# Kernel tuning notes

Hardware: AMD Instinct MI355X
Metric: run time of the kernel (lower is better)

The kernel has to match this reference:

```python
import jax, jax.numpy as jnp
import numpy as np
from functools import partial

B, C, FD, H, W = 8, 256, 128, 64, 64
POSC = 34  # 32 learned pos channels + 2 raw meshgrid channels


def create_meshgrid(h, w):
    # kornia-style normalized grid in [-1, 1], returned as [1, 2, h, w] (x, y)
    xs = jnp.linspace(-1.0, 1.0, w, dtype=jnp.float32)
    ys = jnp.linspace(-1.0, 1.0, h, dtype=jnp.float32)
    gy, gx = jnp.meshgrid(ys, xs, indexing='ij')
    return jnp.stack([gx, gy], axis=0)[None]  # [1,2,h,w]


def conv1x1(x, w, b):
    return jnp.einsum('bchw,oc->bohw', x, w) + b[None, :, None, None]


def pos_gen(feat, pg_w1, pg_b1, pg_w2, pg_b2):
    # PosGen type=2 with detach: two 1x1 'mul' layers (conv + ReLU, no norm)
    b, c, h, w = feat.shape
    feat = jax.lax.stop_gradient(feat)
    pos = jnp.broadcast_to(create_meshgrid(h, w), (b, 2, h, w))
    inp = jnp.concatenate([pos + 1.0, feat], axis=1)           # [b, feat_dim+2, h, w]
    h1 = jax.nn.relu(conv1x1(inp, pg_w1, pg_b1))               # [b, feat_dim, h, w]
    h2 = jax.nn.relu(conv1x1(h1, pg_w2, pg_b2))                # [b, 32, h, w]
    return jnp.concatenate([h2, pos], axis=1)                  # [b, 34, h, w]


def fuser(x, feat, w1, b1, w2, b2):
    # fuser_1D: concat along channels, 1x1 -> hidden (ReLU) -> 1x1 -> 256
    z = jnp.concatenate([x, feat], axis=1)
    z = jax.nn.relu(conv1x1(z, w1, b1))
    return conv1x1(z, w2, b2)


def conv_y(y, dw_w, dw_b, pw_w, pw_b):
    # BasicDWLayer: depthwise 3x3 + pointwise 1x1, no norm, no activation
    z = jax.lax.conv_general_dilated(
        y, dw_w, window_strides=(1, 1), padding='SAME',
        feature_group_count=y.shape[1],
        dimension_numbers=('NCHW', 'OIHW', 'NCHW')) + dw_b[None, :, None, None]
    return conv1x1(z, pw_w, pw_b)


def matching_forward(x, y, feat1, feat2,
                     pg_w1, pg_b1, pg_w2, pg_b2,
                     fus_w1, fus_b1, fus_w2, fus_b2,
                     dw_w, dw_b, pw_w, pw_b,
                     dustbin_vec, dustbin_pos):
    b, c, hx, wx = x.shape
    hy, wy = y.shape[2], y.shape[3]

    posf = pos_gen(feat2, pg_w1, pg_b1, pg_w2, pg_b2)          # [b, 34, hy, wy]
    c_pose = posf.shape[1]
    pos = posf.reshape(b, 1, c_pose, hy * wy).swapaxes(-1, -2)  # [b,1,Nk,34]

    xf = fuser(x, feat1, fus_w1, fus_b1, fus_w2, fus_b2)
    yf = fuser(y, feat2, fus_w1, fus_b1, fus_w2, fus_b2)
    yf = conv_y(yf, dw_w, dw_b, pw_w, pw_b)
    d = yf.shape[1]

    q = xf.reshape(b, 1, d, hx * wx).swapaxes(-1, -2)           # [b,1,Nq,256]
    k = yf.reshape(b, 1, d, hy * wy).swapaxes(-1, -2)           # [b,1,Nk,256]

    # dustbin token augmentation
    k = jnp.concatenate([k, jnp.broadcast_to(dustbin_vec, (b, 1, 1, d))], axis=-2)
    pos = jnp.concatenate([pos, jnp.broadcast_to(dustbin_pos, (b, 1, 1, c_pose))], axis=-2)

    # single-head cross-attention: values are the positional channels
    scores = jnp.einsum('bhqc,bhkc->bhqk', q, k) / jnp.sqrt(jnp.float32(d))
    attn = jax.nn.softmax(scores, axis=-1)
    out = jnp.einsum('bhqk,bhkd->bhqd', attn, pos)              # [b,1,Nq,34]
    return out.swapaxes(-1, -2).reshape(b, c_pose, hx, wx)


def setup_inputs() -> dict:
    key = jax.random.key(0)
    ks = jax.random.split(key, 20)
    s = 0.05
    return {
        'x': jax.random.normal(ks[0], (B, C, H, W), jnp.float32),
        'y': jax.random.normal(ks[1], (B, C, H, W), jnp.float32),
        'feat1': jax.random.normal(ks[2], (B, FD, H, W), jnp.float32),
        'feat2': jax.random.normal(ks[3], (B, FD, H, W), jnp.float32),
        # PosGen type-2 mapping: (feat_dim+2)->feat_dim, feat_dim->(hidden-2=32)
        'pg_w1': jax.random.normal(ks[4], (FD, FD + 2), jnp.float32) * s,
        'pg_b1': jnp.zeros((FD,), jnp.float32),
        'pg_w2': jax.random.normal(ks[5], (32, FD), jnp.float32) * s,
        'pg_b2': jnp.zeros((32,), jnp.float32),
        # fuser_1D: (256+128)->256 hidden, hidden->256
        'fus_w1': jax.random.normal(ks[6], (256, C + FD), jnp.float32) * s,
        'fus_b1': jnp.zeros((256,), jnp.float32),
        'fus_w2': jax.random.normal(ks[7], (C, 256), jnp.float32) * s,
        'fus_b2': jnp.zeros((C,), jnp.float32),
        # conv_y: depthwise 3x3 + pointwise 1x1
        'dw_w': jax.random.normal(ks[8], (C, 1, 3, 3), jnp.float32) * s,
        'dw_b': jnp.zeros((C,), jnp.float32),
        'pw_w': jax.random.normal(ks[9], (C, C), jnp.float32) * s,
        'pw_b': jnp.zeros((C,), jnp.float32),
        'dustbin_vec': jax.random.uniform(ks[10], (1, 1, 1, C), jnp.float32) / 10.0,
        'dustbin_pos': jnp.zeros((1, 1, 1, POSC), jnp.float32) - 10.0,
    }


def reference(x, y, feat1, feat2,
              pg_w1, pg_b1, pg_w2, pg_b2,
              fus_w1, fus_b1, fus_w2, fus_b2,
              dw_w, dw_b, pw_w, pw_b,
              dustbin_vec, dustbin_pos):
    return matching_forward(x, y, feat1, feat2,
                            pg_w1, pg_b1, pg_w2, pg_b2,
                            fus_w1, fus_b1, fus_w2, fus_b2,
                            dw_w, dw_b, pw_w, pw_b,
                            dustbin_vec, dustbin_pos)
```

## Files before the change

kernel.cpp:

```cpp
#include <hip/hip_runtime.h>
#include <hip/hip_bf16.h>

typedef __hip_bfloat16 bf16;
typedef unsigned short ushort_t;
typedef __bf16 bf16x8 __attribute__((ext_vector_type(8)));
typedef float  f32x4  __attribute__((ext_vector_type(4)));

#define HW    4096
#define NB    8
#define KSTR  4160
#define PSTR  4224
#define NTOK  32768
#define QSCALE 0.0901684400557f

__device__ __forceinline__ float lde(const void* p, size_t i, int f32f) {
    return f32f ? ((const float*)p)[i] : (float)((const bf16*)p)[i];
}
__device__ __forceinline__ ushort_t f2bu(float f){ union { __bf16 b; ushort_t u; } cv; cv.b = (__bf16)f; return cv.u; }

__global__ void detect_kernel(const ushort_t* xb, int* flag)
{
    __shared__ int cnt;
    const int t = threadIdx.x;
    if (t == 0) cnt = 0;
    __syncthreads();
    ushort_t h = xb[2*t];
    int e = (h >> 7) & 0xFF;
    if (e >= 133) atomicAdd(&cnt, 1);
    __syncthreads();
    if (t == 0) *flag = (cnt > 8) ? 1 : 0;
}

struct WsPtrs {
    bf16 *fw1t, *fw2t, *pwt, *pgw1t, *pgw2t, *dwt, *pos;
    float *posw, *fb1, *fb2, *pwb, *pgb1, *pgb2, *dwb;
};

__global__ __launch_bounds__(256) void prep_kernel(
    const void* fus_w1, const void* fus_w2, const void* pw_w,
    const void* pg_w1, const void* pg_w2, const void* dw_w,
    const void* fus_b1, const void* fus_b2, const void* pw_b,
    const void* pg_b1, const void* pg_b2, const void* dw_b,
    const void* dpos, WsPtrs W, const int* flag)
{
    const int f = *flag;
    const long n_w1 = 98304, n_w2 = 65536, n_pw = 65536, n_g1 = 16384, n_g2 = 4096;
    const long n_posw = 256, n_dwt = 2304;
    const long n_b = 256, n_gb1 = 128, n_gb2 = 32;
    const long n_mesh = 65536;
    const long n_pad  = 8L*14*PSTR;
    const long n_dust = 272;
    const long n_zt   = 8L*34*127;
    const long total = n_w1+n_w2+n_pw+n_g1+n_g2+n_posw+n_dwt
                     + 3*n_b + n_gb1 + n_gb2 + n_b + n_mesh + n_pad + n_dust + n_zt;

    for (long i = blockIdx.x*256L + threadIdx.x; i < total; i += gridDim.x*256L) {
        long j = i;
        if (j < n_w1) { W.fw1t[j] = __float2bfloat16(lde(fus_w1, j, f)); continue; } j -= n_w1;
        if (j < n_w2) { W.fw2t[j] = __float2bfloat16(lde(fus_w2, j, f)); continue; } j -= n_w2;
        if (j < n_pw) { W.pwt[j]  = __float2bfloat16(lde(pw_w,  j, f)); continue; } j -= n_pw;
        if (j < n_g1) { W.pgw1t[j] = __float2bfloat16(lde(pg_w1, (j>>7)*130 + 2 + (j&127), f)); continue; } j -= n_g1;
        if (j < n_g2) { W.pgw2t[j] = __float2bfloat16(lde(pg_w2, j, f)); continue; } j -= n_g2;
        if (j < n_posw) { W.posw[j] = lde(pg_w1, (j>>1)*130 + (j&1), f); continue; } j -= n_posw;
        if (j < n_dwt) { W.dwt[j] = __float2bfloat16(lde(dw_w, (j&255)*9 + (j>>8), f)); continue; } j -= n_dwt;
        if (j < n_b)   { W.fb1[j] = lde(fus_b1, j, f); continue; } j -= n_b;
        if (j < n_b)   { W.fb2[j] = lde(fus_b2, j, f); continue; } j -= n_b;
        if (j < n_b)   { W.pwb[j] = lde(pw_b, j, f); continue; } j -= n_b;
        if (j < n_gb1) { W.pgb1[j] = lde(pg_b1, j, f); continue; } j -= n_gb1;
        if (j < n_gb2) { W.pgb2[j] = lde(pg_b2, j, f); continue; } j -= n_gb2;
        if (j < n_b)   { W.dwb[j] = lde(dw_b, j, f); continue; } j -= n_b;
        if (j < n_mesh) {
            long b = j >> 13; int rr = (int)((j>>12)&1); int tok = (int)(j & 4095);
            float v = rr ? (-1.f + 2.f*(float)((tok>>6)&63)/63.f)
                         : (-1.f + 2.f*(float)(tok&63)/63.f);
            W.pos[((size_t)b*64 + 32 + rr)*PSTR + tok] = __float2bfloat16(v);
            continue;
        } j -= n_mesh;
        if (j < n_pad) {
            long b = j / (14L*PSTR); long rem = j % (14L*PSTR);
            int row = 34 + (int)(rem / PSTR); int tok = (int)(rem % PSTR);
            float v = (row == 34 && tok <= 4096) ? 1.f : 0.f;
            W.pos[((size_t)b*64 + row)*PSTR + tok] = __float2bfloat16(v);
            continue;
        } j -= n_pad;
        if (j < n_dust) {
            long b = j / 34; int ch = (int)(j % 34);
            W.pos[((size_t)b*64 + ch)*PSTR + 4096] = __float2bfloat16(lde(dpos, ch, f));
            continue;
        } j -= n_dust;
        { long b = j / (34*127); long rem = j % (34*127);
          int ch = (int)(rem / 127); int cc = (int)(rem % 127);
          W.pos[((size_t)b*64 + ch)*PSTR + 4097 + cc] = __float2bfloat16(0.f); }
    }
}

__global__ __launch_bounds__(256) void transpose_kernel(
    const void* main_src, const void* feat_src, bf16* __restrict__ dst, const int* flag)
{
    __shared__ float Tt[64*65];
    const int t = threadIdx.x;
    const int p0 = blockIdx.x * 64;
    const int cht = blockIdx.y;
    const int b = blockIdx.z;
    const int f = *flag;

    const void* src; int ch0, srcC, dc0;
    if (cht < 4) { src = main_src; ch0 = cht*64; srcC = 256; dc0 = ch0; }
    else         { src = feat_src; ch0 = (cht-4)*64; srcC = 128; dc0 = 256 + (cht-4)*64; }

    const int p = t & 63, cq = t >> 6;
    #pragma unroll
    for (int e = 0; e < 16; ++e) {
        int c = e*4 + cq;
        Tt[p*65 + c] = lde(src, ((size_t)b*srcC + ch0 + c)*HW + p0 + p, f);
    }
    __syncthreads();
    const int pr = t >> 2, cs = (t & 3) * 16;
    union { uint4 u4[2]; ushort_t us[16]; } pk;
    #pragma unroll
    for (int u = 0; u < 16; ++u) pk.us[u] = f2bu(Tt[pr*65 + cs + u]);
    ushort_t* op = (ushort_t*)dst + ((size_t)b*HW + p0 + pr)*384 + dc0 + cs;
    *(uint4*)op = pk.u4[0];
    *((uint4*)op + 1) = pk.u4[1];
}

template<int MT, bool RELU, bool POSEPI, int OMODE>
__global__ __launch_bounds__(256) void gemm_mfma(
    const bf16* __restrict__ A, int sa,
    const bf16* __restrict__ Bw, int ldb,
    const float* __restrict__ bias, const float* __restrict__ posw,
    bf16* __restrict__ out, int sm, int K, float oscale)
{
    const int t = threadIdx.x;
    const int w = t >> 6, lane = t & 63;
    const int n = lane & 15, quad = lane >> 4;
    const int p0 = blockIdx.x * 128;
    const int m0 = blockIdx.y * (MT*16);
    const int rowbase = p0 + w*32;

    f32x4 acc[2][MT];
    #pragma unroll
    for (int pt = 0; pt < 2; ++pt)
        #pragma unroll
        for (int mt = 0; mt < MT; ++mt) acc[pt][mt] = (f32x4){0.f,0.f,0.f,0.f};

    const bf16* Ar0 = A + (size_t)(rowbase + n)*sa + quad*8;
    const bf16* Ar1 = A + (size_t)(rowbase + 16 + n)*sa + quad*8;

    bf16x8 a0 = *(const bf16x8*)Ar0;
    bf16x8 a1 = *(const bf16x8*)Ar1;
    bf16x8 bw[MT];
    #pragma unroll
    for (int mt = 0; mt < MT; ++mt)
        bw[mt] = *(const bf16x8*)&Bw[(size_t)(m0 + mt*16 + n)*ldb + quad*8];

    const int kmax = K - 32;
    for (int k0 = 0; k0 < K; k0 += 32) {
        const int kn = (k0 < kmax) ? k0 + 32 : k0;
        bf16x8 na0 = *(const bf16x8*)(Ar0 + kn);
        bf16x8 na1 = *(const bf16x8*)(Ar1 + kn);
        bf16x8 nbw[MT];
        #pragma unroll
        for (int mt = 0; mt < MT; ++mt)
            nbw[mt] = *(const bf16x8*)&Bw[(size_t)(m0 + mt*16 + n)*ldb + kn + quad*8];
        #pragma unroll
        for (int mt = 0; mt < MT; ++mt) {
            acc[0][mt] = __builtin_amdgcn_mfma_f32_16x16x32_bf16(a0, bw[mt], acc[0][mt], 0, 0, 0);
            acc[1][mt] = __builtin_amdgcn_mfma_f32_16x16x32_bf16(a1, bw[mt], acc[1][mt], 0, 0, 0);
        }
        a0 = na0; a1 = na1;
        #pragma unroll
        for (int mt = 0; mt < MT; ++mt) bw[mt] = nbw[mt];
    }

    #pragma unroll
    for (int mt = 0; mt < MT; ++mt) {
        const int m = m0 + mt*16 + n;
        const float bi = bias[m];
        float w0 = 0.f, w1 = 0.f;
        if (POSEPI) { w0 = posw[m*2]; w1 = posw[m*2 + 1]; }
        #pragma unroll
        for (int pt = 0; pt < 2; ++pt) {
            const int tokb = rowbase + pt*16 + quad*4;
            if (OMODE == 1) {
                union { uint2 u2; ushort_t us[4]; } pk;
                #pragma unroll
                for (int r = 0; r < 4; ++r) {
                    float v = acc[pt][mt][r] + bi;
                    if (RELU) v = fmaxf(v, 0.f);
                    pk.us[r] = f2bu(v * oscale);
                }
                size_t oi = ((size_t)(tokb >> 12)*64 + m)*PSTR + (tokb & 4095);
                *(uint2*)((ushort_t*)out + oi) = pk.u2;
            } else {
                #pragma unroll
                for (int r = 0; r < 4; ++r) {
                    int tok = tokb + r;
                    float v = acc[pt][mt][r] + bi;
                    if (POSEPI) {
                        float gx1 = 2.f * (float)(tok & 63) / 63.f;
                        float gy1 = 2.f * (float)((tok >> 6) & 63) / 63.f;
                        v += w0*gx1 + w1*gy1;
                    }
                    if (RELU) v = fmaxf(v, 0.f);
                    v *= oscale;
                    size_t row = (OMODE == 2) ? (size_t)tok + 64*(size_t)(tok >> 12) : (size_t)tok;
                    out[row*sm + m] = __float2bfloat16(v);
                }
            }
        }
    }
}

__global__ __launch_bounds__(256) void dw_kernel(
    const bf16* __restrict__ in, const bf16* __restrict__ dwt,
    const float* __restrict__ dwb, bf16* __restrict__ out)
{
    const int t = threadIdx.x;
    const int tok = blockIdx.x*8 + (t >> 5);
    const int c8 = (t & 31) * 8;
    const int b = tok >> 12, p = tok & 4095;
    const int i = p >> 6, j = p & 63;

    float acc[8];
    #pragma unroll
    for (int u = 0; u < 8; ++u) acc[u] = dwb[c8 + u];

    #pragma unroll
    for (int di = 0; di < 3; ++di) {
        int ii = i + di - 1;
        if (ii < 0 || ii >= 64) continue;
        #pragma unroll
        for (int dj = 0; dj < 3; ++dj) {
            int jj = j + dj - 1;
            if (jj < 0 || jj >= 64) continue;
            int tok2 = (b << 12) + ii*64 + jj;
            bf16x8 xv = *(const bf16x8*)&in[(size_t)tok2*256 + c8];
            bf16x8 wv = *(const bf16x8*)&dwt[(di*3 + dj)*256 + c8];
            #pragma unroll
            for (int u = 0; u < 8; ++u) acc[u] += (float)xv[u] * (float)wv[u];
        }
    }
    union { uint4 u4; ushort_t us[8]; } pk;
    #pragma unroll
    for (int u = 0; u < 8; ++u) pk.us[u] = f2bu(acc[u]);
    *(uint4*)((ushort_t*)out + (size_t)tok*256 + c8) = pk.u4;
}

__global__ __launch_bounds__(256) void fill_late_kernel(
    const void* dvec, bf16* __restrict__ k_t, const int* flag)
{
    const int b = blockIdx.x, t = threadIdx.x;
    k_t[((size_t)b*KSTR + 4096)*256 + t] = __float2bfloat16(lde(dvec, t, *flag));
}

__global__ __launch_bounds__(256, 2) void attn_kernel(
    const bf16* __restrict__ q_t, const bf16* __restrict__ k_t,
    const bf16* __restrict__ pos, void* outv, const int* flag)
{
    __shared__ __align__(16) float red[4*12*64*4];
    __shared__ __align__(16) __bf16 Pb[4*64*40];

    const int t = threadIdx.x;
    const int w = t >> 6, lane = t & 63;
    const int n = lane & 15, quad = lane >> 4;
    const int qt = blockIdx.x, b = blockIdx.y;

    bf16x8 aq[4][8];
    #pragma unroll
    for (int q2 = 0; q2 < 4; ++q2) {
        size_t qrow = (size_t)b*HW + qt*64 + q2*16 + n;
        #pragma unroll
        for (int c = 0; c < 8; ++c)
            aq[q2][c] = *(const bf16x8*)&q_t[qrow*256 + c*32 + quad*8];
    }

    f32x4 pacc[4][3];
    #pragma unroll
    for (int q2 = 0; q2 < 4; ++q2)
        #pragma unroll
        for (int ct = 0; ct < 3; ++ct) pacc[q2][ct] = (f32x4){0.f,0.f,0.f,0.f};

    const bf16* kb0 = k_t + (size_t)b*KSTR*256;
    const bf16* pb0 = pos + (size_t)b*64*PSTR;
    __bf16* Pw = Pb + w*64*40;

    for (int i = 0; i < 33; ++i) {
        const int base = i*128 + w*32;

        #pragma unroll
        for (int nt2 = 0; nt2 < 2; ++nt2) {
            const int kb = base + nt2*16;
            bf16x8 bk[8];
            #pragma unroll
            for (int c = 0; c < 8; ++c)
                bk[c] = *(const bf16x8*)&kb0[(size_t)(kb + n)*256 + c*32 + quad*8];
            f32x4 sacc[4];
            #pragma unroll
            for (int q2 = 0; q2 < 4; ++q2) sacc[q2] = (f32x4){0.f,0.f,0.f,0.f};
            #pragma unroll
            for (int c = 0; c < 8; ++c)
                #pragma unroll
                for (int q2 = 0; q2 < 4; ++q2)
                    sacc[q2] = __builtin_amdgcn_mfma_f32_16x16x32_bf16(aq[q2][c], bk[c], sacc[q2], 0, 0, 0);
            const bool ok = (kb + n) <= 4096;
            #pragma unroll
            for (int q2 = 0; q2 < 4; ++q2)
                #pragma unroll
                for (int r = 0; r < 4; ++r) {
                    float pv = ok ? __builtin_amdgcn_exp2f(sacc[q2][r]) : 0.f;
                    Pw[(q2*16 + quad*4 + r)*40 + nt2*16 + n] = (__bf16)pv;
                }
        }

        bf16x8 bp[3];
        #pragma unroll
        for (int ct = 0; ct < 3; ++ct)
            bp[ct] = *(const bf16x8*)&pb0[(size_t)(ct*16 + n)*PSTR + base + quad*8];

        #pragma unroll
        for (int q2 = 0; q2 < 4; ++q2) {
            bf16x8 aP = *(const bf16x8*)&Pw[(q2*16 + n)*40 + quad*8];
            #pragma unroll
            for (int ct = 0; ct < 3; ++ct)
                pacc[q2][ct] = __builtin_amdgcn_mfma_f32_16x16x32_bf16(aP, bp[ct], pacc[q2][ct], 0, 0, 0);
        }
    }

    #pragma unroll
    for (int q2 = 0; q2 < 4; ++q2)
        #pragma unroll
        for (int ct = 0; ct < 3; ++ct)
            *(f32x4*)&red[(((w*12) + q2*3 + ct)*64 + lane)*4] = pacc[q2][ct];
    __syncthreads();

    f32x4 sum[3];
    #pragma unroll
    for (int ct = 0; ct < 3; ++ct) {
        sum[ct] = (f32x4){0.f,0.f,0.f,0.f};
        #pragma unroll
        for (int w2 = 0; w2 < 4; ++w2) {
            f32x4 v = *(const f32x4*)&red[(((w2*12) + w*3 + ct)*64 + lane)*4];
            sum[ct] += v;
        }
    }
    const int f32o = *flag;
    float linv[4];
    #pragma unroll
    for (int r = 0; r < 4; ++r)
        linv[r] = 1.f / __shfl(sum[2][r], (lane & 48) | 2, 64);
    #pragma unroll
    for (int ct = 0; ct < 3; ++ct) {
        int ch = ct*16 + n;
        if (ch >= 34) continue;
        #pragma unroll
        for (int r = 0; r < 4; ++r) {
            float v = sum[ct][r] * linv[r];
            size_t oi = ((size_t)b*34 + ch)*HW + qt*64 + w*16 + quad*4 + r;
            if (f32o) ((float*)outv)[oi] = v;
            else      ((bf16*)outv)[oi]  = __float2bfloat16(v);
        }
    }
}

extern "C" void kernel_launch(void* const* d_in, const int* in_sizes, int n_in,
                              void* d_out, int out_size, void* d_ws, size_t ws_size,
                              hipStream_t stream)
{
    const void* x      = d_in[0];
    const void* y      = d_in[1];
    const void* feat1  = d_in[2];
    const void* feat2  = d_in[3];
    const void* pg_w1  = d_in[4];
    const void* pg_b1  = d_in[5];
    const void* pg_w2  = d_in[6];
    const void* pg_b2  = d_in[7];
    const void* fus_w1 = d_in[8];
    const void* fus_b1 = d_in[9];
    const void* fus_w2 = d_in[10];
    const void* fus_b2 = d_in[11];
    const void* dw_w   = d_in[12];
    const void* dw_b   = d_in[13];
    const void* pw_w   = d_in[14];
    const void* pw_b   = d_in[15];
    const void* dvec   = d_in[16];
    const void* dpos   = d_in[17];

    char* wsb = (char*)d_ws;
    int*  flag = (int*)wsb;
    size_t off = 16;
    bf16* R1   = (bf16*)(wsb + off); off += (size_t)NTOK*384*2;
    bf16* bufH = (bf16*)(wsb + off); off += (size_t)NTOK*256*2;
    bf16* q_t  = (bf16*)(wsb + off); off += (size_t)NTOK*256*2;
    bf16* pos  = (bf16*)(wsb + off); off += (size_t)NB*64*PSTR*2;
    WsPtrs W;
    W.fw1t  = (bf16*)(wsb + off); off += 98304*2;
    W.fw2t  = (bf16*)(wsb + off); off += 65536*2;
    W.pwt   = (bf16*)(wsb + off); off += 65536*2;
    W.pgw1t = (bf16*)(wsb + off); off += 16384*2;
    W.pgw2t = (bf16*)(wsb + off); off += 4096*2;
    W.dwt   = (bf16*)(wsb + off); off += 2304*2;
    W.pos   = pos;
    W.posw  = (float*)(wsb + off); off += 256*4;
    W.fb1   = (float*)(wsb + off); off += 256*4;
    W.fb2   = (float*)(wsb + off); off += 256*4;
    W.pwb   = (float*)(wsb + off); off += 256*4;
    W.pgb1  = (float*)(wsb + off); off += 128*4;
    W.pgb2  = (float*)(wsb + off); off += 32*4;
    W.dwb   = (float*)(wsb + off); off += 256*4;

    bf16* in_xy = R1;
    bf16* yf    = R1;
    bf16* k_t   = R1;

    dim3 b256(256);

    detect_kernel<<<1, 256, 0, stream>>>((const ushort_t*)x, flag);
    prep_kernel<<<1024, b256, 0, stream>>>(fus_w1, fus_w2, pw_w, pg_w1, pg_w2, dw_w,
                                           fus_b1, fus_b2, pw_b, pg_b1, pg_b2, dw_b,
                                           dpos, W, flag);
    transpose_kernel<<<dim3(64,6,NB), b256, 0, stream>>>(x, feat1, in_xy, flag);
    gemm_mfma<4, true, false, 0><<<dim3(256,4), b256, 0, stream>>>(
        in_xy, 384, W.fw1t, 384, W.fb1, nullptr, bufH, 256, 384, 1.f);
    gemm_mfma<4, false, false, 0><<<dim3(256,4), b256, 0, stream>>>(
        bufH, 256, W.fw2t, 256, W.fb2, nullptr, q_t, 256, 256, QSCALE);
    transpose_kernel<<<dim3(64,6,NB), b256, 0, stream>>>(y, feat2, in_xy, flag);
    gemm_mfma<4, true, true, 0><<<dim3(256,2), b256, 0, stream>>>(
        in_xy + 256, 384, W.pgw1t, 128, W.pgb1, W.posw, bufH, 128, 128, 1.f);
    gemm_mfma<2, true, false, 1><<<dim3(256,1), b256, 0, stream>>>(
        bufH, 128, W.pgw2t, 128, W.pgb2, nullptr, pos, 0, 128, 1.f);
    gemm_mfma<4, true, false, 0><<<dim3(256,4), b256, 0, stream>>>(
        in_xy, 384, W.fw1t, 384, W.fb1, nullptr, bufH, 256, 384, 1.f);
    gemm_mfma<4, false, false, 0><<<dim3(256,4), b256, 0, stream>>>(
        bufH, 256, W.fw2t, 256, W.fb2, nullptr, yf, 256, 256, 1.f);
    dw_kernel<<<dim3(4096), b256, 0, stream>>>(yf, W.dwt, W.dwb, bufH);
    fill_late_kernel<<<dim3(NB), b256, 0, stream>>>(dvec, k_t, flag);
    gemm_mfma<4, false, false, 2><<<dim3(256,4), b256, 0, stream>>>(
        bufH, 256, W.pwt, 256, W.pwb, nullptr, k_t, 256, 256, 1.f);
    attn_kernel<<<dim3(64,NB), b256, 0, stream>>>(q_t, k_t, pos, d_out, flag);
}
```

Baseline: 545.1 us.

## Stage GEMM activations in LDS via async loads and retile attention to 32 queries

The GEMMs become a new kernel that copies a whole token tile (64 or 256 rows) into LDS with global_load_lds and keeps it there, so each activation row is fetched from global memory once instead of once per output-channel block. Row strides are padded (392/264/136) to avoid LDS bank conflicts. The attention kernel now handles 32 queries per block, doubling the grid, and double-buffers the key fragments across iterations. It also shares one LDS buffer between P and the reduction, which lowers LDS use and should raise occupancy. The cost is more register pressure, and the dw kernel writes with padded strides, so the buffers that consume its output must use matching layouts.

```diff
diff --git a/kernel.cpp b/kernel.cpp
--- a/kernel.cpp
+++ b/kernel.cpp
@@ -11,12 +11,21 @@
 #define KSTR  4160
 #define PSTR  4224
 #define NTOK  32768
+#define LDXY  392
+#define LDH   264
+#define LDH1  136
 #define QSCALE 0.0901684400557f
 
 __device__ __forceinline__ float lde(const void* p, size_t i, int f32f) {
     return f32f ? ((const float*)p)[i] : (float)((const bf16*)p)[i];
 }
 __device__ __forceinline__ ushort_t f2bu(float f){ union { __bf16 b; ushort_t u; } cv; cv.b = (__bf16)f; return cv.u; }
+
+__device__ __forceinline__ void async_cp16(const void* g, void* l) {
+    __builtin_amdgcn_global_load_lds(
+        (const __attribute__((address_space(1))) unsigned int*)g,
+        (__attribute__((address_space(3))) unsigned int*)l, 16, 0, 0);
+}
 
 __global__ void detect_kernel(const ushort_t* xb, int* flag)
 {
@@ -119,74 +128,84 @@
     union { uint4 u4[2]; ushort_t us[16]; } pk;
     #pragma unroll
     for (int u = 0; u < 16; ++u) pk.us[u] = f2bu(Tt[pr*65 + cs + u]);
-    ushort_t* op = (ushort_t*)dst + ((size_t)b*HW + p0 + pr)*384 + dc0 + cs;
+    ushort_t* op = (ushort_t*)dst + ((size_t)b*HW + p0 + pr)*LDXY + dc0 + cs;
     *(uint4*)op = pk.u4[0];
     *((uint4*)op + 1) = pk.u4[1];
 }
 
-template<int MT, bool RELU, bool POSEPI, int OMODE>
-__global__ __launch_bounds__(256) void gemm_mfma(
-    const bf16* __restrict__ A, int sa,
+template<int LDA, int MT, bool SPLITM, bool RELU, bool POSEPI, int OMODE>
+__global__ __launch_bounds__(256) void gemm_lds(
+    const bf16* __restrict__ A, int astart, int kiters,
     const bf16* __restrict__ Bw, int ldb,
     const float* __restrict__ bias, const float* __restrict__ posw,
-    bf16* __restrict__ out, int sm, int K, float oscale)
-{
+    bf16* __restrict__ out, int sm, float oscale)
+{
+    constexpr int TB = SPLITM ? 64 : 256;
+    __shared__ __align__(16) __bf16 As[TB*LDA];
+
     const int t = threadIdx.x;
     const int w = t >> 6, lane = t & 63;
     const int n = lane & 15, quad = lane >> 4;
-    const int p0 = blockIdx.x * 128;
-    const int m0 = blockIdx.y * (MT*16);
-    const int rowbase = p0 + w*32;
-
-    f32x4 acc[2][MT];
-    #pragma unroll
-    for (int pt = 0; pt < 2; ++pt)
-        #pragma unroll
-        for (int mt = 0; mt < MT; ++mt) acc[pt][mt] = (f32x4){0.f,0.f,0.f,0.f};
-
-    const bf16* Ar0 = A + (size_t)(rowbase + n)*sa + quad*8;
-    const bf16* Ar1 = A + (size_t)(rowbase + 16 + n)*sa + quad*8;
-
-    bf16x8 a0 = *(const bf16x8*)Ar0;
-    bf16x8 a1 = *(const bf16x8*)Ar1;
-    bf16x8 bw[MT];
+    const int p0 = blockIdx.x * TB;
+
+    constexpr int NI = TB*LDA/512;
+    {
+        const char* gsrc = (const char*)(A + (size_t)p0*LDA);
+        char* ldst = (char*)As;
+        for (int j = w; j < NI; j += 4)
+            async_cp16(gsrc + (size_t)(j*64 + lane)*16, ldst + (size_t)(j*64 + lane)*16);
+    }
+
+    const int wtok = SPLITM ? 0 : w*64;
+    const int wm   = SPLITM ? w*MT*16 : 0;
+
+    f32x4 acc[4][MT];
+    #pragma unroll
+    for (int tt = 0; tt < 4; ++tt)
+        #pragma unroll
+        for (int mt = 0; mt < MT; ++mt) acc[tt][mt] = (f32x4){0.f,0.f,0.f,0.f};
+
+    bf16x8 bf0[MT];
     #pragma unroll
     for (int mt = 0; mt < MT; ++mt)
-        bw[mt] = *(const bf16x8*)&Bw[(size_t)(m0 + mt*16 + n)*ldb + quad*8];
-
-    const int kmax = K - 32;
-    for (int k0 = 0; k0 < K; k0 += 32) {
-        const int kn = (k0 < kmax) ? k0 + 32 : k0;
-        bf16x8 na0 = *(const bf16x8*)(Ar0 + kn);
-        bf16x8 na1 = *(const bf16x8*)(Ar1 + kn);
-        bf16x8 nbw[MT];
+        bf0[mt] = *(const bf16x8*)&Bw[(size_t)(wm + mt*16 + n)*ldb + quad*8];
+
+    __syncthreads();
+
+    for (int ki = 0; ki < kiters; ++ki) {
+        const int k0 = ki*32;
+        const int kn = (ki + 1 < kiters) ? k0 + 32 : k0;
+        bf16x8 bfn[MT];
         #pragma unroll
         for (int mt = 0; mt < MT; ++mt)
-            nbw[mt] = *(const bf16x8*)&Bw[(size_t)(m0 + mt*16 + n)*ldb + kn + quad*8];
-        #pragma unroll
-        for (int mt = 0; mt < MT; ++mt) {
-            acc[0][mt] = __builtin_amdgcn_mfma_f32_16x16x32_bf16(a0, bw[mt], acc[0][mt], 0, 0, 0);
-            acc[1][mt] = __builtin_amdgcn_mfma_f32_16x16x32_bf16(a1, bw[mt], acc[1][mt], 0, 0, 0);
-        }
-        a0 = na0; a1 = na1;
-        #pragma unroll
-        for (int mt = 0; mt < MT; ++mt) bw[mt] = nbw[mt];
+            bfn[mt] = *(const bf16x8*)&Bw[(size_t)(wm + mt*16 + n)*ldb + kn + quad*8];
+        bf16x8 af[4];
+        #pragma unroll
+        for (int tt = 0; tt < 4; ++tt)
+            af[tt] = *(const bf16x8*)&As[(size_t)(wtok + tt*16 + n)*LDA + astart + k0 + quad*8];
+        #pragma unroll
+        for (int tt = 0; tt < 4; ++tt)
+            #pragma unroll
+            for (int mt = 0; mt < MT; ++mt)
+                acc[tt][mt] = __builtin_amdgcn_mfma_f32_16x16x32_bf16(af[tt], bf0[mt], acc[tt][mt], 0, 0, 0);
+        #pragma unroll
+        for (int mt = 0; mt < MT; ++mt) bf0[mt] = bfn[mt];
     }
 
     #pragma unroll
     for (int mt = 0; mt < MT; ++mt) {
-        const int m = m0 + mt*16 + n;
+        const int m = wm + mt*16 + n;
         const float bi = bias[m];
         float w0 = 0.f, w1 = 0.f;
         if (POSEPI) { w0 = posw[m*2]; w1 = posw[m*2 + 1]; }
         #pragma unroll
-        for (int pt = 0; pt < 2; ++pt) {
-            const int tokb = rowbase + pt*16 + quad*4;
+        for (int tt = 0; tt < 4; ++tt) {
+            const int tokb = p0 + wtok + tt*16 + quad*4;
             if (OMODE == 1) {
                 union { uint2 u2; ushort_t us[4]; } pk;
                 #pragma unroll
                 for (int r = 0; r < 4; ++r) {
-                    float v = acc[pt][mt][r] + bi;
+                    float v = acc[tt][mt][r] + bi;
                     if (RELU) v = fmaxf(v, 0.f);
                     pk.us[r] = f2bu(v * oscale);
                 }
@@ -196,7 +215,7 @@
                 #pragma unroll
                 for (int r = 0; r < 4; ++r) {
                     int tok = tokb + r;
-                    float v = acc[pt][mt][r] + bi;
+                    float v = acc[tt][mt][r] + bi;
                     if (POSEPI) {
                         float gx1 = 2.f * (float)(tok & 63) / 63.f;
                         float gy1 = 2.f * (float)((tok >> 6) & 63) / 63.f;
@@ -235,7 +254,7 @@
             int jj = j + dj - 1;
             if (jj < 0 || jj >= 64) continue;
             int tok2 = (b << 12) + ii*64 + jj;
-            bf16x8 xv = *(const bf16x8*)&in[(size_t)tok2*256 + c8];
+            bf16x8 xv = *(const bf16x8*)&in[(size_t)tok2*LDH + c8];
             bf16x8 wv = *(const bf16x8*)&dwt[(di*3 + dj)*256 + c8];
             #pragma unroll
             for (int u = 0; u < 8; ++u) acc[u] += (float)xv[u] * (float)wv[u];
@@ -244,7 +263,7 @@
     union { uint4 u4; ushort_t us[8]; } pk;
     #pragma unroll
     for (int u = 0; u < 8; ++u) pk.us[u] = f2bu(acc[u]);
-    *(uint4*)((ushort_t*)out + (size_t)tok*256 + c8) = pk.u4;
+    *(uint4*)((ushort_t*)out + (size_t)tok*LDH + c8) = pk.u4;
 }
 
 __global__ __launch_bounds__(256) void fill_late_kernel(
@@ -258,68 +277,95 @@
     const bf16* __restrict__ q_t, const bf16* __restrict__ k_t,
     const bf16* __restrict__ pos, void* outv, const int* flag)
 {
-    __shared__ __align__(16) float red[4*12*64*4];
-    __shared__ __align__(16) __bf16 Pb[4*64*40];
+    __shared__ __align__(16) char smem[24576];
+    float*  red = (float*)smem;
+    __bf16* Pb  = (__bf16*)smem;
 
     const int t = threadIdx.x;
     const int w = t >> 6, lane = t & 63;
     const int n = lane & 15, quad = lane >> 4;
-    const int qt = blockIdx.x, b = blockIdx.y;
-
-    bf16x8 aq[4][8];
-    #pragma unroll
-    for (int q2 = 0; q2 < 4; ++q2) {
-        size_t qrow = (size_t)b*HW + qt*64 + q2*16 + n;
+    const int qb = blockIdx.x, b = blockIdx.y;
+
+    bf16x8 aq[2][8];
+    #pragma unroll
+    for (int q2 = 0; q2 < 2; ++q2) {
+        size_t qrow = (size_t)b*HW + qb*32 + q2*16 + n;
         #pragma unroll
         for (int c = 0; c < 8; ++c)
             aq[q2][c] = *(const bf16x8*)&q_t[qrow*256 + c*32 + quad*8];
     }
 
-    f32x4 pacc[4][3];
-    #pragma unroll
-    for (int q2 = 0; q2 < 4; ++q2)
+    f32x4 pacc[2][3];
+    #pragma unroll
+    for (int q2 = 0; q2 < 2; ++q2)
         #pragma unroll
         for (int ct = 0; ct < 3; ++ct) pacc[q2][ct] = (f32x4){0.f,0.f,0.f,0.f};
 
     const bf16* kb0 = k_t + (size_t)b*KSTR*256;
     const bf16* pb0 = pos + (size_t)b*64*PSTR;
-    __bf16* Pw = Pb + w*64*40;
+    __bf16* Pw = Pb + w*32*40;
+
+    bf16x8 bkA[8], bkB[8];
+    #pragma unroll
+    for (int c = 0; c < 8; ++c)
+        bkA[c] = *(const bf16x8*)&kb0[(size_t)(w*32 + n)*256 + c*32 + quad*8];
 
     for (int i = 0; i < 33; ++i) {
         const int base = i*128 + w*32;
 
         #pragma unroll
-        for (int nt2 = 0; nt2 < 2; ++nt2) {
-            const int kb = base + nt2*16;
-            bf16x8 bk[8];
-            #pragma unroll
-            for (int c = 0; c < 8; ++c)
-                bk[c] = *(const bf16x8*)&kb0[(size_t)(kb + n)*256 + c*32 + quad*8];
-            f32x4 sacc[4];
-            #pragma unroll
-            for (int q2 = 0; q2 < 4; ++q2) sacc[q2] = (f32x4){0.f,0.f,0.f,0.f};
-            #pragma unroll
-            for (int c = 0; c < 8; ++c)
-                #pragma unroll
-                for (int q2 = 0; q2 < 4; ++q2)
-                    sacc[q2] = __builtin_amdgcn_mfma_f32_16x16x32_bf16(aq[q2][c], bk[c], sacc[q2], 0, 0, 0);
-            const bool ok = (kb + n) <= 4096;
-            #pragma unroll
-            for (int q2 = 0; q2 < 4; ++q2)
+        for (int c = 0; c < 8; ++c)
+            bkB[c] = *(const bf16x8*)&kb0[(size_t)(base + 16 + n)*256 + c*32 + quad*8];
+
+        f32x4 s0[2] = {{0.f,0.f,0.f,0.f},{0.f,0.f,0.f,0.f}};
+        #pragma unroll
+        for (int c = 0; c < 8; ++c)
+            #pragma unroll
+            for (int q2 = 0; q2 < 2; ++q2)
+                s0[q2] = __builtin_amdgcn_mfma_f32_16x16x32_bf16(aq[q2][c], bkA[c], s0[q2], 0, 0, 0);
+
+        bf16x8 bp[3];
+        #pragma unroll
+        for (int ct = 0; ct < 3; ++ct)
+            bp[ct] = *(const bf16x8*)&pb0[(size_t)(ct*16 + n)*PSTR + base + quad*8];
+
+        {
+            const bool ok = (base + n) <= 4096;
+            #pragma unroll
+            for (int q2 = 0; q2 < 2; ++q2)
                 #pragma unroll
                 for (int r = 0; r < 4; ++r) {
-                    float pv = ok ? __builtin_amdgcn_exp2f(sacc[q2][r]) : 0.f;
-                    Pw[(q2*16 + quad*4 + r)*40 + nt2*16 + n] = (__bf16)pv;
+                    float pv = ok ? __builtin_amdgcn_exp2f(s0[q2][r]) : 0.f;
+                    Pw[(q2*16 + quad*4 + r)*40 + n] = (__bf16)pv;
                 }
         }
 
-        bf16x8 bp[3];
-        #pragma unroll
-        for (int ct = 0; ct < 3; ++ct)
-            bp[ct] = *(const bf16x8*)&pb0[(size_t)(ct*16 + n)*PSTR + base + quad*8];
-
-        #pragma unroll
-        for (int q2 = 0; q2 < 4; ++q2) {
+        f32x4 s1[2] = {{0.f,0.f,0.f,0.f},{0.f,0.f,0.f,0.f}};
+        #pragma unroll
+        for (int c = 0; c < 8; ++c)
+            #pragma unroll
+            for (int q2 = 0; q2 < 2; ++q2)
+                s1[q2] = __builtin_amdgcn_mfma_f32_16x16x32_bf16(aq[q2][c], bkB[c], s1[q2], 0, 0, 0);
+
+        if (i < 32) {
+            #pragma unroll
+            for (int c = 0; c < 8; ++c)
+                bkA[c] = *(const bf16x8*)&kb0[(size_t)(base + 128 + n)*256 + c*32 + quad*8];
+        }
+
+        {
+            const bool ok = (base + 16 + n) <= 4096;
+            #pragma unroll
+            for (int q2 = 0; q2 < 2; ++q2)
+                #pragma unroll
+                for (int r = 0; r < 4; ++r) {
+                    float pv = ok ? __builtin_amdgcn_exp2f(s1[q2][r]) : 0.f;
+                    Pw[(q2*16 + quad*4 + r)*40 + 16 + n] = (__bf16)pv;
+                }
+        }
+
+        #pragma unroll
+        for (int q2 = 0; q2 < 2; ++q2) {
             bf16x8 aP = *(const bf16x8*)&Pw[(q2*16 + n)*40 + quad*8];
             #pragma unroll
             for (int ct = 0; ct < 3; ++ct)
@@ -327,38 +373,39 @@
         }
     }
 
-    #pragma unroll
-    for (int q2 = 0; q2 < 4; ++q2)
+    __syncthreads();
+    #pragma unroll
+    for (int q2 = 0; q2 < 2; ++q2)
         #pragma unroll
         for (int ct = 0; ct < 3; ++ct)
-            *(f32x4*)&red[(((w*12) + q2*3 + ct)*64 + lane)*4] = pacc[q2][ct];
-    __syncthreads();
-
-    f32x4 sum[3];
-    #pragma unroll
-    for (int ct = 0; ct < 3; ++ct) {
-        sum[ct] = (f32x4){0.f,0.f,0.f,0.f};
-        #pragma unroll
-        for (int w2 = 0; w2 < 4; ++w2) {
-            f32x4 v = *(const f32x4*)&red[(((w2*12) + w*3 + ct)*64 + lane)*4];
-            sum[ct] += v;
-        }
-    }
-    const int f32o = *flag;
-    float linv[4];
-    #pragma unroll
-    for (int r = 0; r < 4; ++r)
-        linv[r] = 1.f / __shfl(sum[2][r], (lane & 48) | 2, 64);
-    #pragma unroll
-    for (int ct = 0; ct < 3; ++ct) {
-        int ch = ct*16 + n;
-        if (ch >= 34) continue;
-        #pragma unroll
-        for (int r = 0; r < 4; ++r) {
-            float v = sum[ct][r] * linv[r];
-            size_t oi = ((size_t)b*34 + ch)*HW + qt*64 + w*16 + quad*4 + r;
-            if (f32o) ((float*)outv)[oi] = v;
-            else      ((bf16*)outv)[oi]  = __float2bfloat16(v);
+            *(f32x4*)&red[((w*6 + q2*3 + ct)*64 + lane)*4] = pacc[q2][ct];
+    __syncthreads();
+
+    if (w < 2) {
+        f32x4 sum[3];
+        #pragma unroll
+        for (int ct = 0; ct < 3; ++ct) {
+            sum[ct] = (f32x4){0.f,0.f,0.f,0.f};
+            #pragma unroll
+            for (int w2 = 0; w2 < 4; ++w2)
+                sum[ct] += *(const f32x4*)&red[((w2*6 + w*3 + ct)*64 + lane)*4];
+        }
+        const int f32o = *flag;
+        float linv[4];
+        #pragma unroll
+        for (int r = 0; r < 4; ++r)
+            linv[r] = 1.f / __shfl(sum[2][r], (lane & 48) | 2, 64);
+        #pragma unroll
+        for (int ct = 0; ct < 3; ++ct) {
+            int ch = ct*16 + n;
+            if (ch >= 34) continue;
+            #pragma unroll
+            for (int r = 0; r < 4; ++r) {
+                float v = sum[ct][r] * linv[r];
+                size_t oi = ((size_t)b*34 + ch)*HW + qb*32 + w*16 + quad*4 + r;
+                if (f32o) ((float*)outv)[oi] = v;
+                else      ((bf16*)outv)[oi]  = __float2bfloat16(v);
+            }
         }
     }
 }
@@ -389,8 +436,8 @@
     char* wsb = (char*)d_ws;
     int*  flag = (int*)wsb;
     size_t off = 16;
-    bf16* R1   = (bf16*)(wsb + off); off += (size_t)NTOK*384*2;
-    bf16* bufH = (bf16*)(wsb + off); off += (size_t)NTOK*256*2;
+    bf16* R1   = (bf16*)(wsb + off); off += (size_t)NTOK*LDXY*2;
+    bf16* bufH = (bf16*)(wsb + off); off += (size_t)NTOK*LDH*2;
     bf16* q_t  = (bf16*)(wsb + off); off += (size_t)NTOK*256*2;
     bf16* pos  = (bf16*)(wsb + off); off += (size_t)NB*64*PSTR*2;
     WsPtrs W;
@@ -420,22 +467,22 @@
                                            fus_b1, fus_b2, pw_b, pg_b1, pg_b2, dw_b,
                                            dpos, W, flag);
     transpose_kernel<<<dim3(64,6,NB), b256, 0, stream>>>(x, feat1, in_xy, flag);
-    gemm_mfma<4, true, false, 0><<<dim3(256,4), b256, 0, stream>>>(
-        in_xy, 384, W.fw1t, 384, W.fb1, nullptr, bufH, 256, 384, 1.f);
-    gemm_mfma<4, false, false, 0><<<dim3(256,4), b256, 0, stream>>>(
-        bufH, 256, W.fw2t, 256, W.fb2, nullptr, q_t, 256, 256, QSCALE);
+    gemm_lds<LDXY,4,true,true,false,0><<<dim3(512), b256, 0, stream>>>(
+        in_xy, 0, 12, W.fw1t, 384, W.fb1, nullptr, bufH, LDH, 1.f);
+    gemm_lds<LDH,4,true,false,false,0><<<dim3(512), b256, 0, stream>>>(
+        bufH, 0, 8, W.fw2t, 256, W.fb2, nullptr, q_t, 256, QSCALE);
     transpose_kernel<<<dim3(64,6,NB), b256, 0, stream>>>(y, feat2, in_xy, flag);
-    gemm_mfma<4, true, true, 0><<<dim3(256,2), b256, 0, stream>>>(
-        in_xy + 256, 384, W.pgw1t, 128, W.pgb1, W.posw, bufH, 128, 128, 1.f);
-    gemm_mfma<2, true, false, 1><<<dim3(256,1), b256, 0, stream>>>(
-        bufH, 128, W.pgw2t, 128, W.pgb2, nullptr, pos, 0, 128, 1.f);
-    gemm_mfma<4, true, false, 0><<<dim3(256,4), b256, 0, stream>>>(
-        in_xy, 384, W.fw1t, 384, W.fb1, nullptr, bufH, 256, 384, 1.f);
-    gemm_mfma<4, false, false, 0><<<dim3(256,4), b256, 0, stream>>>(
-        bufH, 256, W.fw2t, 256, W.fb2, nullptr, yf, 256, 256, 1.f);
+    gemm_lds<LDXY,2,true,true,true,0><<<dim3(512), b256, 0, stream>>>(
+        in_xy, 256, 4, W.pgw1t, 128, W.pgb1, W.posw, bufH, LDH1, 1.f);
+    gemm_lds<LDH1,2,false,true,false,1><<<dim3(128), b256, 0, stream>>>(
+        bufH, 0, 4, W.pgw2t, 128, W.pgb2, nullptr, pos, 0, 1.f);
+    gemm_lds<LDXY,4,true,true,false,0><<<dim3(512), b256, 0, stream>>>(
+        in_xy, 0, 12, W.fw1t, 384, W.fb1, nullptr, bufH, LDH, 1.f);
+    gemm_lds<LDH,4,true,false,false,0><<<dim3(512), b256, 0, stream>>>(
+        bufH, 0, 8, W.fw2t, 256, W.fb2, nullptr, yf, LDH, 1.f);
     dw_kernel<<<dim3(4096), b256, 0, stream>>>(yf, W.dwt, W.dwb, bufH);
     fill_late_kernel<<<dim3(NB), b256, 0, stream>>>(dvec, k_t, flag);
-    gemm_mfma<4, false, false, 2><<<dim3(256,4), b256, 0, stream>>>(
-        bufH, 256, W.pwt, 256, W.pwb, nullptr, k_t, 256, 256, 1.f);
-    attn_kernel<<<dim3(64,NB), b256, 0, stream>>>(q_t, k_t, pos, d_out, flag);
-}
+    gemm_lds<LDH,4,true,false,false,2><<<dim3(512), b256, 0, stream>>>(
+        bufH, 0, 8, W.pwt, 256, W.pwb, nullptr, k_t, 256, 1.f);
+    attn_kernel<<<dim3(128,NB), b256, 0, stream>>>(q_t, k_t, pos, d_out, flag);
+}
```

Result: slower. 604.0 us (+10.8%).
